# Optimization experiments

Measured on AMD Instinct MI355X. Metric: run time of the kernel, lower is better.

## Reference

```python
import jax, jax.numpy as jnp
import numpy as np

QK = 64
KNN = 16
EPS = 1e-5


def conv1(x, w, b):
    # x: (B,C,N), w: (O,C) -> (B,O,N)
    return jnp.einsum('oc,bcn->bon', w, x) + b[None, :, None]


def conv2(x, w, b):
    # x: (B,C,N,k), w: (O,C) -> (B,O,N,k)
    return jnp.einsum('oc,bcnk->bonk', w, x) + b[None, :, None, None]


def bn1(x, g, b, m, v):
    return g[None, :, None] * (x - m[None, :, None]) * jax.lax.rsqrt(v + EPS)[None, :, None] + b[None, :, None]


def bn2(x, g, b, m, v):
    return g[None, :, None, None] * (x - m[None, :, None, None]) * jax.lax.rsqrt(v + EPS)[None, :, None, None] + b[None, :, None, None]


def gather_nk(t, idx):
    # t: (B,C,M), idx: (B,N,k) -> (B,C,N,k)
    return jax.vmap(lambda tb, ib: tb[:, ib])(t, idx)


def setup_inputs():
    key = jax.random.key(0)
    ks = jax.random.split(key, 40)
    B, N, M = 2, 16384, 4096
    w = lambda k, s: jax.random.normal(k, s, dtype=jnp.float32) * 0.05
    d = {}
    d['xyz_hr'] = jax.random.normal(ks[0], (B, 3, N), dtype=jnp.float32)
    d['xyz_lr'] = jax.random.normal(ks[1], (B, 3, M), dtype=jnp.float32)
    d['sft_feat_lr'] = jax.random.normal(ks[2], (B, 6, M), dtype=jnp.float32)
    d['val_lr'] = jax.random.normal(ks[3], (B, 64, M), dtype=jnp.float32)
    # geom_encoder: Conv1d(3,64) -> BN -> ReLU -> Conv1d(64,64)
    d['ge_w1'] = w(ks[4], (QK, 3)); d['ge_b1'] = w(ks[5], (QK,))
    d['ge_g1'] = jnp.ones((QK,)); d['ge_be1'] = jnp.zeros((QK,))
    d['ge_m1'] = w(ks[6], (QK,)); d['ge_v1'] = jax.random.uniform(ks[7], (QK,), minval=0.5, maxval=1.5)
    d['ge_w2'] = w(ks[8], (QK, QK)); d['ge_b2'] = w(ks[9], (QK,))
    # scale/shift convs Conv1d(6,64)
    d['sc_w'] = w(ks[10], (QK, 6)); d['sc_b'] = w(ks[11], (QK,))
    d['sh_w'] = w(ks[12], (QK, 6)); d['sh_b'] = w(ks[13], (QK,))
    # sem query/key Conv1d(64,64)
    d['q_w'] = w(ks[14], (QK, QK)); d['q_b'] = w(ks[15], (QK,))
    d['k_w'] = w(ks[16], (QK, QK)); d['k_b'] = w(ks[17], (QK,))
    # bdy_head: Conv1d(64,64) -> BN -> ReLU -> Conv1d(64,1) -> Sigmoid
    d['bd_w1'] = w(ks[18], (64, QK)); d['bd_b1'] = w(ks[19], (64,))
    d['bd_g'] = jnp.ones((64,)); d['bd_be'] = jnp.zeros((64,))
    d['bd_m'] = w(ks[20], (64,)); d['bd_v'] = jax.random.uniform(ks[21], (64,), minval=0.5, maxval=1.5)
    d['bd_w2'] = w(ks[22], (1, 64)); d['bd_b2'] = w(ks[23], (1,))
    # rel_pos_mlp: Conv2d(3,64) -> BN2d -> ReLU -> Conv2d(64,64)
    d['rp_w1'] = w(ks[24], (QK, 3)); d['rp_b1'] = w(ks[25], (QK,))
    d['rp_g'] = jnp.ones((QK,)); d['rp_be'] = jnp.zeros((QK,))
    d['rp_m'] = w(ks[26], (QK,)); d['rp_v'] = jax.random.uniform(ks[27], (QK,), minval=0.5, maxval=1.5)
    d['rp_w2'] = w(ks[28], (QK, QK)); d['rp_b2'] = w(ks[29], (QK,))
    return d


def reference(xyz_hr, xyz_lr, sft_feat_lr, val_lr,
              ge_w1, ge_b1, ge_g1, ge_be1, ge_m1, ge_v1, ge_w2, ge_b2,
              sc_w, sc_b, sh_w, sh_b, q_w, q_b, k_w, k_b,
              bd_w1, bd_b1, bd_g, bd_be, bd_m, bd_v, bd_w2, bd_b2,
              rp_w1, rp_b1, rp_g, rp_be, rp_m, rp_v, rp_w2, rp_b2):
    B, _, M = sft_feat_lr.shape
    curr_k = min(KNN, M)

    def geom_enc(x):
        h = jax.nn.relu(bn1(conv1(x, ge_w1, ge_b1), ge_g1, ge_be1, ge_m1, ge_v1))
        return conv1(h, ge_w2, ge_b2)

    geom_hr = geom_enc(xyz_hr)                     # (B,64,N)
    geom_lr = geom_enc(xyz_lr)                     # (B,64,M)
    scale = conv1(sft_feat_lr, sc_w, sc_b)
    shift = conv1(sft_feat_lr, sh_w, sh_b)
    geom_lr_mod = geom_lr * (scale + 1.0) + shift
    Q = conv1(geom_hr, q_w, q_b)                   # (B,64,N)
    K = conv1(geom_lr_mod, k_w, k_b)               # (B,64,M)
    # boundary head
    h = jax.nn.relu(bn1(conv1(geom_hr, bd_w1, bd_b1), bd_g, bd_be, bd_m, bd_v))
    bdy_prob = jax.nn.sigmoid(conv1(h, bd_w2, bd_b2))  # (B,1,N)
    # kNN via squared distances (same argmin ordering as torch.cdist)
    hr_t = jnp.swapaxes(xyz_hr, 1, 2)              # (B,N,3)
    lr_t = jnp.swapaxes(xyz_lr, 1, 2)              # (B,M,3)
    d2 = (jnp.sum(hr_t**2, -1)[:, :, None] + jnp.sum(lr_t**2, -1)[:, None, :]
          - 2.0 * jnp.einsum('bnd,bmd->bnm', hr_t, lr_t))  # (B,N,M)
    _, k_idx = jax.lax.top_k(-d2, curr_k)          # (B,N,k) int32
    k_idx = jax.lax.stop_gradient(k_idx)

    K_g = gather_nk(K, k_idx)                      # (B,64,N,k)
    xyz_lr_g = gather_nk(xyz_lr, k_idx)            # (B,3,N,k)
    rel_pos = xyz_hr[:, :, :, None] - xyz_lr_g     # (B,3,N,k)
    pe = jax.nn.relu(bn2(conv2(rel_pos, rp_w1, rp_b1), rp_g, rp_be, rp_m, rp_v))
    pos_enc = conv2(pe, rp_w2, rp_b2)              # (B,64,N,k)
    logits = jnp.sum(Q[:, :, :, None] * (K_g + pos_enc), axis=1) / np.sqrt(QK)  # (B,N,k)
    attn = jax.nn.softmax(logits, axis=-1)
    val_g = gather_nk(val_lr, k_idx)               # (B,Cv,N,k)
    out = jnp.sum(attn[:, None, :, :] * val_g, axis=-1)  # (B,Cv,N)
    return out, bdy_prob
```

## Files before the change

kernel.cpp:

```cpp
#include <hip/hip_runtime.h>
#include <hip/hip_bf16.h>

#define B_ 2
#define N_ 16384
#define M_ 4096
#define EPS_ 1e-5f

typedef float f32x2 __attribute__((ext_vector_type(2)));
typedef float f32x4 __attribute__((ext_vector_type(4)));

__device__ __forceinline__ float b2f(const __hip_bfloat16 v) { return __bfloat162float(v); }

__device__ __forceinline__ float ldin(const void* p, size_t i, int f32) {
    return f32 ? ((const float*)p)[i] : __bfloat162float(((const __hip_bfloat16*)p)[i]);
}
__device__ __forceinline__ void stout(void* o, size_t i, float v, int f32) {
    if (f32) ((float*)o)[i] = v;
    else     ((__hip_bfloat16*)o)[i] = __float2bfloat16(v);
}

__device__ __forceinline__ float d2np(float x, float y, float z, float hn, float4 q) {
    float dot = __fadd_rn(__fadd_rn(__fmul_rn(x, q.x), __fmul_rn(y, q.y)), __fmul_rn(z, q.z));
    return __fsub_rn(__fadd_rn(hn, q.w), __fmul_rn(2.f, dot));
}
__device__ __forceinline__ float norm3np(float x, float y, float z) {
    return __fadd_rn(__fadd_rn(__fmul_rn(x, x), __fmul_rn(y, y)), __fmul_rn(z, z));
}

#define O_GE_W1 0
#define O_GE_B1 192
#define O_GE_W2 256
#define O_GE_B2 4352
#define O_QW    4416
#define O_QB    8512
#define O_KW    8576
#define O_KB    12672
#define O_SCW   12736
#define O_SCB   13120
#define O_SHW   13184
#define O_SHB   13568
#define O_BDW1  13632
#define O_BDB1  17728
#define O_BDW2  17792
#define O_BDB2  17856
#define O_RPW1  17920
#define O_RPB1  18112
#define O_RPW2  18176
#define O_RPB2  22272
#define OB_LR    92160
#define OB_Q     223232
#define OB_KT    4417536
#define OB_VT    5466112
#define OB_KIDX  6514688
#define OB_DFLAG 7694336
#define OB_PA1   7563264
#define OB_PA2   7628800
#define O_T_GE_W2 1923840
#define O_T_QW    1927936
#define O_T_KW    1932032
#define O_T_BDW1  1936128

#define TMAX 256

__global__ __launch_bounds__(256) void prep_kernel(
    const void* xyz_hr,
    const void* ge_w1, const void* ge_b1, const void* ge_g1, const void* ge_be1,
    const void* ge_m1, const void* ge_v1, const void* ge_w2, const void* ge_b2,
    const void* sc_w, const void* sc_b, const void* sh_w, const void* sh_b,
    const void* q_w, const void* q_b, const void* k_w, const void* k_b,
    const void* bd_w1, const void* bd_b1, const void* bd_g, const void* bd_be,
    const void* bd_m, const void* bd_v, const void* bd_w2, const void* bd_b2,
    const void* rp_w1, const void* rp_b1, const void* rp_g, const void* rp_be,
    const void* rp_m, const void* rp_v, const void* rp_w2, const void* rp_b2,
    float* W, int* dflag)
{
    __shared__ int scnt;
    int t = threadIdx.x;
    if (t == 0) scnt = 0;
    __syncthreads();
    if (t < 128) {
        unsigned short u = ((const unsigned short*)xyz_hr)[t];
        int e = (u >> 7) & 0xFF;
        int ok = (e >= 113 && e <= 132) || ((u & 0x7FFF) == 0);
        if (ok) atomicAdd(&scnt, 1);
    }
    __syncthreads();
    const int f32 = (scnt < 110) ? 1 : 0;
    if (t == 0) *dflag = f32;

    if (t < 64) {
        float s = ldin(ge_g1, t, f32) * rsqrtf(ldin(ge_v1, t, f32) + EPS_);
        for (int d = 0; d < 3; ++d) W[O_GE_W1 + t*3 + d] = s * ldin(ge_w1, t*3 + d, f32);
        W[O_GE_B1 + t] = s * (ldin(ge_b1, t, f32) - ldin(ge_m1, t, f32)) + ldin(ge_be1, t, f32);
        W[O_GE_B2 + t] = ldin(ge_b2, t, f32);
        W[O_QB + t] = ldin(q_b, t, f32);
        W[O_KB + t] = ldin(k_b, t, f32);
        W[O_SCB + t] = ldin(sc_b, t, f32);
        W[O_SHB + t] = ldin(sh_b, t, f32);
        float sb = ldin(bd_g, t, f32) * rsqrtf(ldin(bd_v, t, f32) + EPS_);
        W[O_BDB1 + t] = sb * (ldin(bd_b1, t, f32) - ldin(bd_m, t, f32)) + ldin(bd_be, t, f32);
        W[O_BDW2 + t] = ldin(bd_w2, t, f32);
        float sr = ldin(rp_g, t, f32) * rsqrtf(ldin(rp_v, t, f32) + EPS_);
        for (int d = 0; d < 3; ++d) W[O_RPW1 + t*3 + d] = sr * ldin(rp_w1, t*3 + d, f32);
        W[O_RPB1 + t] = sr * (ldin(rp_b1, t, f32) - ldin(rp_m, t, f32)) + ldin(rp_be, t, f32);
        W[O_RPB2 + t] = ldin(rp_b2, t, f32);
    }
    if (t == 0) W[O_BDB2] = ldin(bd_b2, 0, f32);
    for (int i = t; i < 4096; i += 256) {
        int c = i >> 6, r = i & 63;
        float w2 = ldin(ge_w2, i, f32);
        float qw = ldin(q_w, i, f32);
        float kw = ldin(k_w, i, f32);
        float sb = ldin(bd_g, c, f32) * rsqrtf(ldin(bd_v, c, f32) + EPS_);
        float bw = sb * ldin(bd_w1, i, f32);
        W[O_GE_W2 + i] = w2;
        W[O_QW + i]    = qw;
        W[O_KW + i]    = kw;
        W[O_RPW2 + i]  = ldin(rp_w2, i, f32);
        W[O_BDW1 + i]  = bw;
        W[O_T_GE_W2 + r*64 + c] = w2;
        W[O_T_QW    + r*64 + c] = qw;
        W[O_T_KW    + r*64 + c] = kw;
        W[O_T_BDW1  + r*64 + c] = bw;
    }
    for (int i = t; i < 384; i += 256) {
        W[O_SCW + i] = ldin(sc_w, i, f32);
        W[O_SHW + i] = ldin(sh_w, i, f32);
    }
}

__global__ __launch_bounds__(256) void lr_kernel(
    const void* __restrict__ xyz_lr,
    const void* __restrict__ sft,
    const void* __restrict__ val,
    const float* __restrict__ W,
    __hip_bfloat16* __restrict__ Kt, __hip_bfloat16* __restrict__ Vt,
    float4* __restrict__ LR, float* __restrict__ PA1, float* __restrict__ PA2,
    const int* dflag)
{
    const int f32 = *dflag;
    int lane = threadIdx.x & 63;
    int p = blockIdx.x * 4 + (threadIdx.x >> 6);
    int b = p >> 12, m = p & (M_ - 1);
    size_t base = (size_t)b*3*M_ + m;
    float x = ldin(xyz_lr, base, f32), y = ldin(xyz_lr, base + M_, f32), z = ldin(xyz_lr, base + 2*M_, f32);
    if (lane == 0) {
        float hn = norm3np(x, y, z);
        LR[p] = make_float4(x, y, z, hn);
        int k = m >> 1, o = m & 1;
        float* a1 = PA1 + ((size_t)b*2048 + k)*4;
        float* a2 = PA2 + ((size_t)b*2048 + k)*4;
        a1[o] = x; a1[2+o] = y;
        a2[o] = z; a2[2+o] = hn;
    }

    const float* w1 = W + O_GE_W1 + lane*3;
    float h = fmaxf(fmaf(w1[2], z, fmaf(w1[1], y, fmaf(w1[0], x, W[O_GE_B1 + lane]))), 0.f);
    float g = W[O_GE_B2 + lane];
#pragma unroll
    for (int i = 0; i < 64; ++i) {
        g = fmaf(W[O_T_GE_W2 + i*64 + lane], __shfl(h, i, 64), g);
    }
    float sc = W[O_SCB + lane], sh = W[O_SHB + lane];
    const float* wsc = W + O_SCW + lane*6;
    const float* wsh = W + O_SHW + lane*6;
#pragma unroll
    for (int d = 0; d < 6; ++d) {
        float s6 = ldin(sft, (size_t)b*6*M_ + d*M_ + m, f32);
        sc = fmaf(wsc[d], s6, sc); sh = fmaf(wsh[d], s6, sh);
    }
    float mod = fmaf(g, sc + 1.f, sh);
    float k = W[O_KB + lane];
#pragma unroll
    for (int i = 0; i < 64; ++i) {
        k = fmaf(W[O_T_KW + i*64 + lane], __shfl(mod, i, 64), k);
    }
    Kt[(size_t)p*64 + lane] = __float2bfloat16(k);
    Vt[(size_t)p*64 + lane] = __float2bfloat16(ldin(val, (size_t)b*64*M_ + (size_t)lane*M_ + m, f32));
}

__global__ __launch_bounds__(256) void hr_kernel(
    const void* __restrict__ xyz_hr,
    const float* __restrict__ W,
    __hip_bfloat16* __restrict__ Q,
    void* __restrict__ out, const int* dflag)
{
    const int f32 = *dflag;
    int lane = threadIdx.x & 63;
    int p = blockIdx.x * 4 + (threadIdx.x >> 6);
    int b = p >> 14, n = p & (N_ - 1);
    size_t base = (size_t)b*3*N_ + n;
    float x = ldin(xyz_hr, base, f32), y = ldin(xyz_hr, base + N_, f32), z = ldin(xyz_hr, base + 2*N_, f32);

    const float* w1 = W + O_GE_W1 + lane*3;
    float h = fmaxf(fmaf(w1[2], z, fmaf(w1[1], y, fmaf(w1[0], x, W[O_GE_B1 + lane]))), 0.f);
    float g = W[O_GE_B2 + lane];
#pragma unroll
    for (int i = 0; i < 64; ++i) {
        g = fmaf(W[O_T_GE_W2 + i*64 + lane], __shfl(h, i, 64), g);
    }
    float q = W[O_QB + lane];
#pragma unroll
    for (int i = 0; i < 64; ++i) {
        q = fmaf(W[O_T_QW + i*64 + lane], __shfl(g, i, 64), q);
    }
    Q[(size_t)p*64 + lane] = __float2bfloat16(q);
    float hb = W[O_BDB1 + lane];
#pragma unroll
    for (int i = 0; i < 64; ++i) {
        hb = fmaf(W[O_T_BDW1 + i*64 + lane], __shfl(g, i, 64), hb);
    }
    float o = W[O_BDW2 + lane] * fmaxf(hb, 0.f);
#pragma unroll
    for (int sh = 1; sh < 64; sh <<= 1) o += __shfl_xor(o, sh, 64);
    if (lane == 0) {
        o += W[O_BDB2];
        stout(out, (size_t)B_*64*N_ + (size_t)b*N_ + n, 1.f / (1.f + __expf(-o)), f32);
    }
}

#define CE(da, ia, db, ib) { \
    bool sw_ = (db < da) || (db == da && ib < ia); \
    float td_ = da; int ti_ = ia; \
    da = sw_ ? db : da; ia = sw_ ? ib : ia; \
    db = sw_ ? td_ : db; ib = sw_ ? ti_ : ib; }

__device__ __forceinline__ void topk_insert(float (&bd)[16], int (&bi)[16], float d2, int m) {
    if (d2 < bd[15] || (d2 == bd[15] && m < bi[15])) {
        bd[15] = d2; bi[15] = m;
#pragma unroll
        for (int j = 15; j > 0; --j) CE(bd[j-1], bi[j-1], bd[j], bi[j]);
    }
}

__device__ __forceinline__ int lesslex(uint2 e, float cd, int ci) {
    float dj = __uint_as_float(e.x);
    int   ij = (int)e.y;
    return (dj < cd || (dj == cd && ij < ci)) ? 1 : 0;
}

__global__ __launch_bounds__(256, 4) void knn_kernel(
    const void* __restrict__ xyz_hr,
    const float4* __restrict__ LR,
    const f32x4* __restrict__ PA1, const f32x4* __restrict__ PA2,
    unsigned short* __restrict__ kidx, const int* dflag)
{
#pragma clang fp reassociate(off)
#pragma clang fp contract(off)
    __shared__ uint2 scand[4 * TMAX];
    __shared__ f32x4 sP1[256];
    __shared__ f32x4 sP2[256];
    const int f32 = *dflag;
    int t    = threadIdx.x;
    int lane = t & 63;
    int wid  = t >> 6;
    int p = blockIdx.x * 4 + wid;
    int b = p >> 14, n = p & (N_ - 1);
    size_t base = (size_t)b*3*N_ + n;
    float x = ldin(xyz_hr, base, f32), y = ldin(xyz_hr, base + N_, f32), z = ldin(xyz_hr, base + 2*N_, f32);
    float hn = norm3np(x, y, z);
    const float4* L = LR + b*M_;
    const f32x4* P1 = PA1 + (size_t)b*2048;
    const f32x4* P2 = PA2 + (size_t)b*2048;

    f32x2 d2p[32];
    f32x2 xx = {x, x}, yy = {y, y}, zz = {z, z}, hh = {hn, hn};
    const f32x2 m2 = {-2.f, -2.f};
    const f32x2 inf2 = {3.4e38f, 3.4e38f};
    f32x2 vm0 = inf2, vm1 = inf2, vm2 = inf2, vm3 = inf2;
#pragma unroll
    for (int c = 0; c < 8; ++c) {
        __syncthreads();
        sP1[t] = P1[c*256 + t];
        sP2[t] = P2[c*256 + t];
        __syncthreads();
#pragma unroll
        for (int i = 0; i < 4; ++i) {
            f32x4 a  = sP1[lane + i*64];
            f32x4 bb = sP2[lane + i*64];
            f32x2 qx = __builtin_shufflevector(a,  a,  0, 1);
            f32x2 qy = __builtin_shufflevector(a,  a,  2, 3);
            f32x2 qz = __builtin_shufflevector(bb, bb, 0, 1);
            f32x2 qw = __builtin_shufflevector(bb, bb, 2, 3);
            f32x2 dot = ((xx*qx) + (yy*qy)) + (zz*qz);
            f32x2 d2  = __builtin_elementwise_fma(m2, dot, hh + qw);
            d2p[c*4 + i] = d2;
            if (i == 0) vm0 = __builtin_elementwise_min(vm0, d2);
            if (i == 1) vm1 = __builtin_elementwise_min(vm1, d2);
            if (i == 2) vm2 = __builtin_elementwise_min(vm2, d2);
            if (i == 3) vm3 = __builtin_elementwise_min(vm3, d2);
        }
    }
    f32x2 vm = __builtin_elementwise_min(__builtin_elementwise_min(vm0, vm1),
                                         __builtin_elementwise_min(vm2, vm3));
    float v = fminf(vm.x, vm.y);
    v = fminf(v, __shfl_xor(v, 16, 64));
    v = fminf(v, __shfl_xor(v, 32, 64));
    float tau = v;
#pragma unroll
    for (int st = 1; st <= 8; st <<= 1) tau = fmaxf(tau, __shfl_xor(tau, st, 64));

    int cnt = 0;
#pragma unroll
    for (int j = 0; j < 32; ++j)
        cnt += ((d2p[j].x <= tau) ? 1 : 0) + ((d2p[j].y <= tau) ? 1 : 0);
    int inc = cnt;
#pragma unroll
    for (int st = 1; st < 64; st <<= 1) {
        int o = __shfl_up(inc, st, 64);
        if (lane >= st) inc += o;
    }
    int off = inc - cnt;
    int T = __shfl(inc, 63, 64);

    if (T > TMAX) {
        float bd[16]; int bi[16];
#pragma unroll
        for (int j = 0; j < 16; ++j) { bd[j] = 3.4e38f; bi[j] = 0x7fffffff; }
        for (int m = 0; m < M_; ++m) {
            topk_insert(bd, bi, d2np(x, y, z, hn, L[m]), m);
        }
        if (lane == 0) {
            unsigned short* kr = kidx + (size_t)p*16;
#pragma unroll
            for (int j = 0; j < 16; ++j) kr[j] = (unsigned short)bi[j];
        }
        return;
    }

    uint2* wc = scand + wid * TMAX;
#pragma unroll
    for (int j = 0; j < 32; ++j) {
        int m0 = 2*lane + 128*j;
        if (d2p[j].x <= tau) { wc[off] = make_uint2(__float_as_uint(d2p[j].x), (unsigned)m0);     off++; }
        if (d2p[j].y <= tau) { wc[off] = make_uint2(__float_as_uint(d2p[j].y), (unsigned)(m0+1)); off++; }
    }
    int Tp = (T + 3) & ~3;
    if (lane < Tp - T) wc[T + lane] = make_uint2(0x7f800000u, 0xffffu);
    asm volatile("s_waitcnt lgkmcnt(0)" ::: "memory");

    for (int t2 = lane; t2 < T; t2 += 64) {
        uint2 cv = wc[t2];
        float cd = __uint_as_float(cv.x);
        int   ci = (int)cv.y;
        int rank = 0;
        for (int j = 0; j < Tp; j += 4) {
            uint2 e0 = wc[j], e1 = wc[j+1], e2 = wc[j+2], e3 = wc[j+3];
            rank += lesslex(e0, cd, ci) + lesslex(e1, cd, ci)
                  + lesslex(e2, cd, ci) + lesslex(e3, cd, ci);
        }
        if (rank < 16) kidx[(size_t)p*16 + rank] = (unsigned short)ci;
    }
}

__global__ __launch_bounds__(256) void attn_kernel(
    const void* __restrict__ xyz_hr,
    const float4* __restrict__ LR,
    const float* __restrict__ W,
    const __hip_bfloat16* __restrict__ Q,
    const __hip_bfloat16* __restrict__ Kt,
    const __hip_bfloat16* __restrict__ Vt,
    const unsigned short* __restrict__ kidx,
    void* __restrict__ out, const int* dflag)
{
    const int f32 = *dflag;
    int p = (blockIdx.x * 256 + threadIdx.x) >> 6;
    int lane = threadIdx.x & 63;
    float fw0 = W[O_RPW1 + lane*3], fw1 = W[O_RPW1 + lane*3 + 1], fw2 = W[O_RPW1 + lane*3 + 2];
    float fb  = W[O_RPB1 + lane];

    int b = p >> 14, n = p & (N_ - 1);
    size_t base = (size_t)b*3*N_ + n;
    float xh = ldin(xyz_hr, base, f32), yh = ldin(xyz_hr, base + N_, f32), zh = ldin(xyz_hr, base + 2*N_, f32);
    float qc = b2f(Q[(size_t)p*64 + lane]);
    float q2 = 0.f;
#pragma unroll
    for (int cc = 0; cc < 64; ++cc) {
        float qb = __shfl(qc, cc, 64);
        q2 = fmaf(W[O_RPW2 + cc*64 + lane], qb, q2);
    }
    int idxv = (int)kidx[(size_t)p*16 + (lane & 15)];
    const float4* L = LR + b*M_;
    const __hip_bfloat16* Ktb = Kt + (size_t)b*M_*64;
    const __hip_bfloat16* Vtb = Vt + (size_t)b*M_*64;
    float lg[16];
#pragma unroll
    for (int j = 0; j < 16; ++j) {
        int mj = __shfl(idxv, j, 64);
        mj = (mj < M_) ? mj : (M_ - 1);
        float4 pl = L[mj];
        float r0 = xh - pl.x, r1 = yh - pl.y, r2 = zh - pl.z;
        float pe = fmaxf(fmaf(fw2, r2, fmaf(fw1, r1, fmaf(fw0, r0, fb))), 0.f);
        float v = fmaf(qc, b2f(Ktb[(size_t)mj*64 + lane]), q2 * pe);
#pragma unroll
        for (int sh = 1; sh < 64; sh <<= 1) v += __shfl_xor(v, sh, 64);
        lg[j] = v * 0.125f;
    }
    float mx = lg[0];
#pragma unroll
    for (int j = 1; j < 16; ++j) mx = fmaxf(mx, lg[j]);
    float sum = 0.f;
#pragma unroll
    for (int j = 0; j < 16; ++j) { lg[j] = __expf(lg[j] - mx); sum += lg[j]; }
    float inv = 1.f / sum;
    float o = 0.f;
#pragma unroll
    for (int j = 0; j < 16; ++j) {
        int mj = __shfl(idxv, j, 64);
        mj = (mj < M_) ? mj : (M_ - 1);
        o = fmaf(lg[j] * inv, b2f(Vtb[(size_t)mj*64 + lane]), o);
    }
    stout(out, ((size_t)(b*64 + lane))*N_ + n, o, f32);
}

extern "C" void kernel_launch(void* const* d_in, const int* in_sizes, int n_in,
                              void* d_out, int out_size, void* d_ws, size_t ws_size,
                              hipStream_t stream) {
    const void* xyz_hr = d_in[0];
    const void* xyz_lr = d_in[1];
    const void* sft    = d_in[2];
    const void* val    = d_in[3];

    char* ws = (char*)d_ws;
    float* W  = (float*)ws;
    float4* LR = (float4*)(ws + OB_LR);
    __hip_bfloat16* Qp = (__hip_bfloat16*)(ws + OB_Q);
    __hip_bfloat16* Kt = (__hip_bfloat16*)(ws + OB_KT);
    __hip_bfloat16* Vt = (__hip_bfloat16*)(ws + OB_VT);
    unsigned short* kidx = (unsigned short*)(ws + OB_KIDX);
    float* PA1 = (float*)(ws + OB_PA1);
    float* PA2 = (float*)(ws + OB_PA2);
    int* dflag = (int*)(ws + OB_DFLAG);

    prep_kernel<<<1, 256, 0, stream>>>(
        xyz_hr,
        d_in[4],  d_in[5],  d_in[6],  d_in[7],  d_in[8],  d_in[9],  d_in[10], d_in[11],
        d_in[12], d_in[13], d_in[14], d_in[15], d_in[16], d_in[17], d_in[18], d_in[19],
        d_in[20], d_in[21], d_in[22], d_in[23], d_in[24], d_in[25], d_in[26], d_in[27],
        d_in[28], d_in[29], d_in[30], d_in[31], d_in[32], d_in[33], d_in[34], d_in[35],
        W, dflag);
    lr_kernel<<<2048, 256, 0, stream>>>(xyz_lr, sft, val, W, Kt, Vt, LR, PA1, PA2, dflag);
    hr_kernel<<<8192, 256, 0, stream>>>(xyz_hr, W, Qp, d_out, dflag);
    knn_kernel<<<8192, 256, 0, stream>>>(xyz_hr, LR, (const f32x4*)PA1, (const f32x4*)PA2, kidx, dflag);
    attn_kernel<<<8192, 256, 0, stream>>>(xyz_hr, LR, W, Qp, Kt, Vt, kidx, d_out, dflag);
}
```

Before: 384.9 us.

## Recompute distances in second pass with LDS atomics instead of register cache

Drops the 64-register per-thread cache of squared distances and instead recomputes them in a second sweep over the staged LR chunks. Candidates under the threshold are appended through shared-memory atomic counters rather than a wave-wide prefix scan. Launch bounds are raised to 8 blocks per SM to use the lower register pressure. The cost is twice the distance arithmetic and shared-memory staging, plus serialised LDS atomics per candidate. Candidate order in the buffer becomes nondeterministic, which the rank-based selection tolerates.

```diff
diff --git a/kernel.cpp b/kernel.cpp
--- a/kernel.cpp
+++ b/kernel.cpp
@@ -239,7 +239,7 @@
     return (dj < cd || (dj == cd && ij < ci)) ? 1 : 0;
 }
 
-__global__ __launch_bounds__(256, 4) void knn_kernel(
+__global__ __launch_bounds__(256, 8) void knn_kernel(
     const void* __restrict__ xyz_hr,
     const float4* __restrict__ LR,
     const f32x4* __restrict__ PA1, const f32x4* __restrict__ PA2,
@@ -250,6 +250,7 @@
     __shared__ uint2 scand[4 * TMAX];
     __shared__ f32x4 sP1[256];
     __shared__ f32x4 sP2[256];
+    __shared__ int   wcnt[4];
     const int f32 = *dflag;
     int t    = threadIdx.x;
     int lane = t & 63;
@@ -262,12 +263,13 @@
     const float4* L = LR + b*M_;
     const f32x4* P1 = PA1 + (size_t)b*2048;
     const f32x4* P2 = PA2 + (size_t)b*2048;
-
-    f32x2 d2p[32];
+    if (t < 4) wcnt[t] = 0;
+
     f32x2 xx = {x, x}, yy = {y, y}, zz = {z, z}, hh = {hn, hn};
     const f32x2 m2 = {-2.f, -2.f};
     const f32x2 inf2 = {3.4e38f, 3.4e38f};
-    f32x2 vm0 = inf2, vm1 = inf2, vm2 = inf2, vm3 = inf2;
+
+    f32x2 vm0 = inf2, vm1 = inf2;
 #pragma unroll
     for (int c = 0; c < 8; ++c) {
         __syncthreads();
@@ -284,34 +286,48 @@
             f32x2 qw = __builtin_shufflevector(bb, bb, 2, 3);
             f32x2 dot = ((xx*qx) + (yy*qy)) + (zz*qz);
             f32x2 d2  = __builtin_elementwise_fma(m2, dot, hh + qw);
-            d2p[c*4 + i] = d2;
-            if (i == 0) vm0 = __builtin_elementwise_min(vm0, d2);
-            if (i == 1) vm1 = __builtin_elementwise_min(vm1, d2);
-            if (i == 2) vm2 = __builtin_elementwise_min(vm2, d2);
-            if (i == 3) vm3 = __builtin_elementwise_min(vm3, d2);
+            if ((i & 1) == 0) vm0 = __builtin_elementwise_min(vm0, d2);
+            else              vm1 = __builtin_elementwise_min(vm1, d2);
         }
     }
-    f32x2 vm = __builtin_elementwise_min(__builtin_elementwise_min(vm0, vm1),
-                                         __builtin_elementwise_min(vm2, vm3));
-    float v = fminf(vm.x, vm.y);
+    f32x2 vmv = __builtin_elementwise_min(vm0, vm1);
+    float v = fminf(vmv.x, vmv.y);
     v = fminf(v, __shfl_xor(v, 16, 64));
     v = fminf(v, __shfl_xor(v, 32, 64));
     float tau = v;
 #pragma unroll
     for (int st = 1; st <= 8; st <<= 1) tau = fmaxf(tau, __shfl_xor(tau, st, 64));
 
-    int cnt = 0;
-#pragma unroll
-    for (int j = 0; j < 32; ++j)
-        cnt += ((d2p[j].x <= tau) ? 1 : 0) + ((d2p[j].y <= tau) ? 1 : 0);
-    int inc = cnt;
-#pragma unroll
-    for (int st = 1; st < 64; st <<= 1) {
-        int o = __shfl_up(inc, st, 64);
-        if (lane >= st) inc += o;
-    }
-    int off = inc - cnt;
-    int T = __shfl(inc, 63, 64);
+    uint2* wc = scand + wid * TMAX;
+#pragma unroll
+    for (int c = 0; c < 8; ++c) {
+        __syncthreads();
+        sP1[t] = P1[c*256 + t];
+        sP2[t] = P2[c*256 + t];
+        __syncthreads();
+#pragma unroll
+        for (int i = 0; i < 4; ++i) {
+            f32x4 a  = sP1[lane + i*64];
+            f32x4 bb = sP2[lane + i*64];
+            f32x2 qx = __builtin_shufflevector(a,  a,  0, 1);
+            f32x2 qy = __builtin_shufflevector(a,  a,  2, 3);
+            f32x2 qz = __builtin_shufflevector(bb, bb, 0, 1);
+            f32x2 qw = __builtin_shufflevector(bb, bb, 2, 3);
+            f32x2 dot = ((xx*qx) + (yy*qy)) + (zz*qz);
+            f32x2 d2  = __builtin_elementwise_fma(m2, dot, hh + qw);
+            int m0 = 2*lane + 512*c + 128*i;
+            if (d2.x <= tau) {
+                int o = atomicAdd(&wcnt[wid], 1);
+                if (o < TMAX) wc[o] = make_uint2(__float_as_uint(d2.x), (unsigned)m0);
+            }
+            if (d2.y <= tau) {
+                int o = atomicAdd(&wcnt[wid], 1);
+                if (o < TMAX) wc[o] = make_uint2(__float_as_uint(d2.y), (unsigned)(m0+1));
+            }
+        }
+    }
+    asm volatile("s_waitcnt lgkmcnt(0)" ::: "memory");
+    int T = wcnt[wid];
 
     if (T > TMAX) {
         float bd[16]; int bi[16];
@@ -328,13 +344,6 @@
         return;
     }
 
-    uint2* wc = scand + wid * TMAX;
-#pragma unroll
-    for (int j = 0; j < 32; ++j) {
-        int m0 = 2*lane + 128*j;
-        if (d2p[j].x <= tau) { wc[off] = make_uint2(__float_as_uint(d2p[j].x), (unsigned)m0);     off++; }
-        if (d2p[j].y <= tau) { wc[off] = make_uint2(__float_as_uint(d2p[j].y), (unsigned)(m0+1)); off++; }
-    }
     int Tp = (T + 3) & ~3;
     if (lane < Tp - T) wc[T + lane] = make_uint2(0x7f800000u, 0xffffu);
     asm volatile("s_waitcnt lgkmcnt(0)" ::: "memory");
```

Result: slower. 393.8 us (+2.3%).
